# Kernel optimization log

Measured on AMD Instinct MI355X. Metric: run time of the kernel, lower is better.

Reference implementation:

```python
import jax, jax.numpy as jnp
import numpy as np

B, D, C = 8192, 2048, 1000
EPS32 = float(np.finfo(np.float32).eps)      # torch clamp_probs uses finfo.eps
LOG_2PI = float(np.log(2.0 * np.pi))
GAMMA = float(1.0 / np.exp(100.0))           # lerp at global_step=0 -> start_val = 1/exp(start_rho)


def setup_inputs() -> dict:
    key = jax.random.key(0)
    k = jax.random.split(key, 6)
    feature = jax.random.normal(k[0], (B, D), jnp.float32)
    target = jax.random.randint(k[1], (B,), 0, C)
    eps = jax.random.normal(k[2], (B, D), jnp.float32)
    # y_project: Linear(C, D) -> weight [D, C], bias [D]
    y_w = jax.random.normal(k[3], (D, C), jnp.float32) * 0.02
    y_b = jnp.zeros((D,), jnp.float32)
    # cls_project: Linear(D, C) -> weight [C, D], bias [C]
    # small weights + positive bias keep Categorical probs positive (torch would
    # clamp negatives to eps; we replicate the clamp but avoid degenerate NaNs)
    cls_w = jax.random.normal(k[4], (C, D), jnp.float32) * 0.001
    cls_b = jnp.ones((C,), jnp.float32) * 5.0
    return dict(feature=feature, y_w=y_w, y_b=y_b, cls_w=cls_w, cls_b=cls_b,
                eps=eps, target=target)


def reference(feature, y_w, y_b, cls_w, cls_b, eps, target):
    # z = m.sample() : identity-covariance MVN sample, detached (torch .sample())
    z = jax.lax.stop_gradient(feature + eps)                      # [B, D]

    # y_emb = y_project(one_hot(target)) == gather of weight columns + bias
    y_emb = jnp.take(y_w, target, axis=1).T + y_b                 # [B, D]

    # Categorical(probs=cls_project(z)): normalize, clamp, log
    probs_raw = z @ cls_w.T + cls_b                               # [B, C]
    p = probs_raw / jnp.sum(probs_raw, axis=-1, keepdims=True)
    logits = jnp.log(jnp.clip(p, EPS32, 1.0 - EPS32))             # [B, C]

    # identity-covariance MVN log_prob in closed form
    const = 0.5 * D * LOG_2PI
    h1 = 0.5 * jnp.sum((z - feature) ** 2, axis=-1) + const       # -m.log_prob(z)
    h2 = 0.5 * jnp.sum((z - y_emb) ** 2, axis=-1) + const         # -y_emb_d.log_prob(z)
    h3 = -jnp.take_along_axis(logits, target[:, None], axis=1)[:, 0]

    rex = h2 - h1
    loss = jnp.mean(jnp.float32(GAMMA) * rex + h3)
    return logits, loss
```

## Files before the change

kernel.cpp:

```cpp
#include <hip/hip_runtime.h>
#include <hip/hip_bf16.h>

#define B_ROWS 8192
#define D_DIM  2048
#define C_DIM  1000
#define C_PAD  1024

#define EPS32   1.1920928955078125e-07f
#define GAMMA_F 3.7200759760208361e-44f

typedef __attribute__((ext_vector_type(8))) short short8;
typedef __attribute__((ext_vector_type(4))) float f32x4;

#define GLOAD_LDS16(gptr, lptr) \
  __builtin_amdgcn_global_load_lds((const __attribute__((address_space(1))) void*)(gptr), \
                                   (__attribute__((address_space(3))) void*)(lptr), 16, 0, 0)

__device__ inline unsigned short f2bf(float x) {
  union { __hip_bfloat16 b; unsigned short u; } cv;
  cv.b = __float2bfloat16(x);
  return cv.u;
}

__device__ inline float wave_red(float v) {
#pragma unroll
  for (int off = 32; off > 0; off >>= 1) v += __shfl_down(v, off, 64);
  return v;
}

__global__ __launch_bounds__(256) void prep(const float* __restrict__ cls_w,
                                            const float* __restrict__ y_w,
                                            const float* __restrict__ y_b,
                                            __hip_bfloat16* __restrict__ clsw_bf,
                                            float* __restrict__ ywtb) {
  __shared__ float tile[32][33];
  int bid = blockIdx.x;
  if (bid < 1024) {
    int j = (bid * 256 + threadIdx.x) * 8;
    int row = j >> 11;
    int col = j & 2047;
    union { unsigned short u[8]; uint4 v; } pk;
    if (row < C_DIM) {
      const float* src = cls_w + (size_t)row * D_DIM + col;
#pragma unroll
      for (int i = 0; i < 8; ++i) pk.u[i] = f2bf(src[i]);
    } else {
#pragma unroll
      for (int i = 0; i < 8; ++i) pk.u[i] = 0;
    }
    *(uint4*)((unsigned short*)clsw_bf + j) = pk.v;
  } else {
    int b2 = bid - 1024;
    int tb = b2 & 31, db = b2 >> 5;
    int t0 = tb * 32, d0 = db * 32;
    int tx = threadIdx.x & 31, ty = threadIdx.x >> 5;
#pragma unroll
    for (int r = 0; r < 4; ++r) {
      int d = d0 + ty + r * 8;
      int t = t0 + tx;
      tile[ty + r * 8][tx] = (t < C_DIM) ? y_w[(size_t)d * C_DIM + t] : 0.f;
    }
    __syncthreads();
#pragma unroll
    for (int r = 0; r < 4; ++r) {
      int t = t0 + ty + r * 8;
      int d = d0 + tx;
      if (t < C_DIM) ywtb[(size_t)t * D_DIM + d] = tile[tx][ty + r * 8] + y_b[d];
    }
  }
}

__global__ __launch_bounds__(256) void fuse_z(const float* __restrict__ feature,
                                              const float* __restrict__ eps,
                                              const float* __restrict__ ywtb,
                                              const int* __restrict__ target,
                                              __hip_bfloat16* __restrict__ z_bf,
                                              float* __restrict__ rex) {
  int b = blockIdx.x;
  int tid = threadIdx.x;
  int t = target[b];
  const float4* f4 = (const float4*)(feature + (size_t)b * D_DIM);
  const float4* e4 = (const float4*)(eps + (size_t)b * D_DIM);
  const float4* y4 = (const float4*)(ywtb + (size_t)t * D_DIM);
  uint2* zrow = (uint2*)((unsigned short*)z_bf + (size_t)b * D_DIM);

  float se = 0.f, sd = 0.f;
#pragma unroll
  for (int i = 0; i < 2; ++i) {
    int idx = tid + i * 256;
    float4 f = f4[idx];
    float4 e = e4[idx];
    float4 y = y4[idx];
    float z0 = f.x + e.x, z1 = f.y + e.y, z2 = f.z + e.z, z3 = f.w + e.w;
    union { unsigned short u[4]; uint2 v; } pz;
    pz.u[0] = f2bf(z0); pz.u[1] = f2bf(z1); pz.u[2] = f2bf(z2); pz.u[3] = f2bf(z3);
    zrow[idx] = pz.v;
    float a0 = z0 - f.x, a1 = z1 - f.y, a2 = z2 - f.z, a3 = z3 - f.w;
    se += a0 * a0 + a1 * a1 + a2 * a2 + a3 * a3;
    float g0 = z0 - y.x, g1 = z1 - y.y, g2 = z2 - y.z, g3 = z3 - y.w;
    sd += g0 * g0 + g1 * g1 + g2 * g2 + g3 * g3;
  }
  se = wave_red(se);
  sd = wave_red(sd);
  __shared__ float s1[4], s2[4];
  int lane = tid & 63, w = tid >> 6;
  if (lane == 0) { s1[w] = se; s2[w] = sd; }
  __syncthreads();
  if (tid == 0) {
    float S1 = s1[0] + s1[1] + s1[2] + s1[3];
    float S2 = s2[0] + s2[1] + s2[2] + s2[3];
    rex[b] = 0.5f * (S2 - S1);
  }
}

__global__ __launch_bounds__(256) void gemm_bt(const __hip_bfloat16* __restrict__ A,
                                               const __hip_bfloat16* __restrict__ Bt,
                                               const float* __restrict__ cls_b,
                                               float* __restrict__ out) {
  __shared__ __align__(16) __hip_bfloat16 sA[64 * 64];
  __shared__ __align__(16) __hip_bfloat16 sB[128 * 64];
  const int tid = threadIdx.x;
  const int m0 = blockIdx.x * 64;
  const int n0 = blockIdx.y * 128;
  const int w = tid >> 6, lane = tid & 63;
  const int wn = w * 32;
  const int l15 = lane & 15, quad = lane >> 4;

  f32x4 acc[4][2] = {};

  for (int k0 = 0; k0 < D_DIM; k0 += 64) {
#pragma unroll
    for (int i = 0; i < 2; ++i) {
      int j = i * 256 + tid;
      int row = j >> 3, cc = j & 7;
      GLOAD_LDS16(A + (size_t)(m0 + row) * D_DIM + k0 + cc * 8, &sA[j * 8]);
    }
#pragma unroll
    for (int i = 0; i < 4; ++i) {
      int j = i * 256 + tid;
      int row = j >> 3, cc = j & 7;
      GLOAD_LDS16(Bt + (size_t)(n0 + row) * D_DIM + k0 + cc * 8, &sB[j * 8]);
    }
    __syncthreads();
#pragma unroll
    for (int kk = 0; kk < 64; kk += 32) {
      short8 af[4], bfr[2];
#pragma unroll
      for (int i = 0; i < 4; ++i)
        af[i] = *(const short8*)&sA[(i * 16 + l15) * 64 + kk + quad * 8];
#pragma unroll
      for (int jn = 0; jn < 2; ++jn)
        bfr[jn] = *(const short8*)&sB[(wn + jn * 16 + l15) * 64 + kk + quad * 8];
#pragma unroll
      for (int i = 0; i < 4; ++i)
#pragma unroll
        for (int jn = 0; jn < 2; ++jn)
          acc[i][jn] = __builtin_amdgcn_mfma_f32_16x16x32_bf16(af[i], bfr[jn], acc[i][jn], 0, 0, 0);
    }
    __syncthreads();
  }

#pragma unroll
  for (int i = 0; i < 4; ++i) {
    int row = m0 + i * 16 + quad * 4;
#pragma unroll
    for (int jn = 0; jn < 2; ++jn) {
      int col = n0 + wn + jn * 16 + l15;
      if (col < C_DIM) {
        float bias = cls_b[col];
#pragma unroll
        for (int r = 0; r < 4; ++r)
          out[(size_t)(row + r) * C_DIM + col] = acc[i][jn][r] + bias;
      }
    }
  }
}

__global__ __launch_bounds__(256) void rownorm(float* __restrict__ out,
                                               const int* __restrict__ target,
                                               float* __restrict__ rowloss) {
  int b = blockIdx.x, tid = threadIdx.x;
  float* row = out + (size_t)b * C_DIM;
  float v[4];
  float s = 0.f;
#pragma unroll
  for (int i = 0; i < 4; ++i) {
    int c = tid + i * 256;
    v[i] = (c < C_DIM) ? row[c] : 0.f;
    s += v[i];
  }
  s = wave_red(s);
  __shared__ float ws_[4];
  __shared__ float h3s;
  int lane = tid & 63, w = tid >> 6;
  if (lane == 0) ws_[w] = s;
  __syncthreads();
  float total = ws_[0] + ws_[1] + ws_[2] + ws_[3];
  float inv = 1.0f / total;
  int t = target[b];
#pragma unroll
  for (int i = 0; i < 4; ++i) {
    int c = tid + i * 256;
    if (c < C_DIM) {
      float p = v[i] * inv;
      p = fminf(fmaxf(p, EPS32), 1.0f - EPS32);
      float lg = __logf(p);
      row[c] = lg;
      if (c == t) h3s = -lg;
    }
  }
  __syncthreads();
  if (tid == 0) {
    float rx = rowloss[b];
    rowloss[b] = fmaf(GAMMA_F, rx, h3s);
  }
}

__global__ __launch_bounds__(256) void finalize(const float* __restrict__ rowloss,
                                                float* __restrict__ out_loss) {
  int tid = threadIdx.x;
  float s = 0.f;
  for (int i = tid; i < B_ROWS; i += 256) s += rowloss[i];
  s = wave_red(s);
  __shared__ float sm[4];
  if ((tid & 63) == 0) sm[tid >> 6] = s;
  __syncthreads();
  if (tid == 0) out_loss[0] = (sm[0] + sm[1] + sm[2] + sm[3]) * (1.0f / B_ROWS);
}

extern "C" void kernel_launch(void* const* d_in, const int* in_sizes, int n_in,
                              void* d_out, int out_size, void* d_ws, size_t ws_size,
                              hipStream_t stream) {
  const float* feature = (const float*)d_in[0];
  const float* y_w     = (const float*)d_in[1];
  const float* y_b     = (const float*)d_in[2];
  const float* cls_w   = (const float*)d_in[3];
  const float* cls_b   = (const float*)d_in[4];
  const float* eps     = (const float*)d_in[5];
  const int*   target  = (const int*)d_in[6];
  float* out = (float*)d_out;

  char* ws = (char*)d_ws;
  __hip_bfloat16* z_bf    = (__hip_bfloat16*)ws;
  __hip_bfloat16* clsw_bf = (__hip_bfloat16*)(ws + 33554432);
  float*          ywtb    = (float*)(ws + 33554432 + 4194304);
  float*          rex     = (float*)(ws + 33554432 + 4194304 + 8192000);

  prep<<<dim3(1024 + 2048), 256, 0, stream>>>(cls_w, y_w, y_b, clsw_bf, ywtb);
  fuse_z<<<dim3(B_ROWS), 256, 0, stream>>>(feature, eps, ywtb, target, z_bf, rex);
  gemm_bt<<<dim3(B_ROWS / 64, C_PAD / 128), 256, 0, stream>>>(z_bf, clsw_bf, cls_b, out);
  rownorm<<<dim3(B_ROWS), 256, 0, stream>>>(out, target, rex);
  finalize<<<dim3(1), 256, 0, stream>>>(rex, out + (size_t)B_ROWS * C_DIM);
}
```

Measured before the change: 262.1 us.

## Enlarge GEMM tile to 128x128 with XOR-swizzled LDS and atomic loss reduction

The GEMM block tile grows from 64x128 to 128x128, with each of the four waves computing a 64x64 sub-tile (4x4 MFMAs). This raises MFMA work per LDS fragment load and halves the number of blocks. LDS chunks are XOR-swizzled by row to cut bank conflicts on the short8 fragment reads. The separate finalize kernel is removed: rownorm atomically adds each row's scaled loss into the output, which prep zeroes first. This saves a launch but makes the float summation order nondeterministic.

```diff
diff --git a/kernel.cpp b/kernel.cpp
--- a/kernel.cpp
+++ b/kernel.cpp
@@ -32,9 +32,11 @@
                                             const float* __restrict__ y_w,
                                             const float* __restrict__ y_b,
                                             __hip_bfloat16* __restrict__ clsw_bf,
-                                            float* __restrict__ ywtb) {
+                                            float* __restrict__ ywtb,
+                                            float* __restrict__ out_loss) {
   __shared__ float tile[32][33];
   int bid = blockIdx.x;
+  if (bid == 0 && threadIdx.x == 0) out_loss[0] = 0.f;
   if (bid < 1024) {
     int j = (bid * 256 + threadIdx.x) * 8;
     int row = j >> 11;
@@ -117,44 +119,47 @@
                                                const __hip_bfloat16* __restrict__ Bt,
                                                const float* __restrict__ cls_b,
                                                float* __restrict__ out) {
-  __shared__ __align__(16) __hip_bfloat16 sA[64 * 64];
+  __shared__ __align__(16) __hip_bfloat16 sA[128 * 64];
   __shared__ __align__(16) __hip_bfloat16 sB[128 * 64];
   const int tid = threadIdx.x;
-  const int m0 = blockIdx.x * 64;
+  const int m0 = blockIdx.x * 128;
   const int n0 = blockIdx.y * 128;
   const int w = tid >> 6, lane = tid & 63;
-  const int wn = w * 32;
+  const int wm = (w & 1) * 64, wn = (w >> 1) * 64;
   const int l15 = lane & 15, quad = lane >> 4;
 
-  f32x4 acc[4][2] = {};
+  f32x4 acc[4][4] = {};
 
   for (int k0 = 0; k0 < D_DIM; k0 += 64) {
-#pragma unroll
-    for (int i = 0; i < 2; ++i) {
-      int j = i * 256 + tid;
-      int row = j >> 3, cc = j & 7;
-      GLOAD_LDS16(A + (size_t)(m0 + row) * D_DIM + k0 + cc * 8, &sA[j * 8]);
-    }
 #pragma unroll
     for (int i = 0; i < 4; ++i) {
       int j = i * 256 + tid;
-      int row = j >> 3, cc = j & 7;
-      GLOAD_LDS16(Bt + (size_t)(n0 + row) * D_DIM + k0 + cc * 8, &sB[j * 8]);
+      int row = j >> 3;
+      int cc = (j & 7) ^ (row & 7);
+      const __hip_bfloat16* srcA = A + (size_t)(m0 + row) * D_DIM + k0 + cc * 8;
+      const __hip_bfloat16* srcB = Bt + (size_t)(n0 + row) * D_DIM + k0 + cc * 8;
+      GLOAD_LDS16(srcA, &sA[j * 8]);
+      GLOAD_LDS16(srcB, &sB[j * 8]);
     }
     __syncthreads();
 #pragma unroll
     for (int kk = 0; kk < 64; kk += 32) {
-      short8 af[4], bfr[2];
+      const int ccr = (kk >> 3) + quad;
+      short8 af[4], bfr[4];
+#pragma unroll
+      for (int i = 0; i < 4; ++i) {
+        int r = wm + i * 16 + l15;
+        af[i] = *(const short8*)&sA[(r * 8 + (ccr ^ (r & 7))) * 8];
+      }
+#pragma unroll
+      for (int jn = 0; jn < 4; ++jn) {
+        int r = wn + jn * 16 + l15;
+        bfr[jn] = *(const short8*)&sB[(r * 8 + (ccr ^ (r & 7))) * 8];
+      }
 #pragma unroll
       for (int i = 0; i < 4; ++i)
-        af[i] = *(const short8*)&sA[(i * 16 + l15) * 64 + kk + quad * 8];
-#pragma unroll
-      for (int jn = 0; jn < 2; ++jn)
-        bfr[jn] = *(const short8*)&sB[(wn + jn * 16 + l15) * 64 + kk + quad * 8];
-#pragma unroll
-      for (int i = 0; i < 4; ++i)
-#pragma unroll
-        for (int jn = 0; jn < 2; ++jn)
+#pragma unroll
+        for (int jn = 0; jn < 4; ++jn)
           acc[i][jn] = __builtin_amdgcn_mfma_f32_16x16x32_bf16(af[i], bfr[jn], acc[i][jn], 0, 0, 0);
     }
     __syncthreads();
@@ -162,9 +167,9 @@
 
 #pragma unroll
   for (int i = 0; i < 4; ++i) {
-    int row = m0 + i * 16 + quad * 4;
-#pragma unroll
-    for (int jn = 0; jn < 2; ++jn) {
+    int row = m0 + wm + i * 16 + quad * 4;
+#pragma unroll
+    for (int jn = 0; jn < 4; ++jn) {
       int col = n0 + wn + jn * 16 + l15;
       if (col < C_DIM) {
         float bias = cls_b[col];
@@ -178,7 +183,8 @@
 
 __global__ __launch_bounds__(256) void rownorm(float* __restrict__ out,
                                                const int* __restrict__ target,
-                                               float* __restrict__ rowloss) {
+                                               const float* __restrict__ rex,
+                                               float* __restrict__ out_loss) {
   int b = blockIdx.x, tid = threadIdx.x;
   float* row = out + (size_t)b * C_DIM;
   float v[4];
@@ -211,21 +217,9 @@
   }
   __syncthreads();
   if (tid == 0) {
-    float rx = rowloss[b];
-    rowloss[b] = fmaf(GAMMA_F, rx, h3s);
-  }
-}
-
-__global__ __launch_bounds__(256) void finalize(const float* __restrict__ rowloss,
-                                                float* __restrict__ out_loss) {
-  int tid = threadIdx.x;
-  float s = 0.f;
-  for (int i = tid; i < B_ROWS; i += 256) s += rowloss[i];
-  s = wave_red(s);
-  __shared__ float sm[4];
-  if ((tid & 63) == 0) sm[tid >> 6] = s;
-  __syncthreads();
-  if (tid == 0) out_loss[0] = (sm[0] + sm[1] + sm[2] + sm[3]) * (1.0f / B_ROWS);
+    float rowloss = fmaf(GAMMA_F, rex[b], h3s);
+    atomicAdd(out_loss, rowloss * (1.0f / B_ROWS));
+  }
 }
 
 extern "C" void kernel_launch(void* const* d_in, const int* in_sizes, int n_in,
@@ -239,6 +233,7 @@
   const float* eps     = (const float*)d_in[5];
   const int*   target  = (const int*)d_in[6];
   float* out = (float*)d_out;
+  float* out_loss = out + (size_t)B_ROWS * C_DIM;
 
   char* ws = (char*)d_ws;
   __hip_bfloat16* z_bf    = (__hip_bfloat16*)ws;
@@ -246,9 +241,8 @@
   float*          ywtb    = (float*)(ws + 33554432 + 4194304);
   float*          rex     = (float*)(ws + 33554432 + 4194304 + 8192000);
 
-  prep<<<dim3(1024 + 2048), 256, 0, stream>>>(cls_w, y_w, y_b, clsw_bf, ywtb);
+  prep<<<dim3(1024 + 2048), 256, 0, stream>>>(cls_w, y_w, y_b, clsw_bf, ywtb, out_loss);
   fuse_z<<<dim3(B_ROWS), 256, 0, stream>>>(feature, eps, ywtb, target, z_bf, rex);
-  gemm_bt<<<dim3(B_ROWS / 64, C_PAD / 128), 256, 0, stream>>>(z_bf, clsw_bf, cls_b, out);
-  rownorm<<<dim3(B_ROWS), 256, 0, stream>>>(out, target, rex);
-  finalize<<<dim3(1), 256, 0, stream>>>(rex, out + (size_t)B_ROWS * C_DIM);
-}
+  gemm_bt<<<dim3(B_ROWS / 128, C_PAD / 128), 256, 0, stream>>>(z_bf, clsw_bf, cls_b, out);
+  rownorm<<<dim3(B_ROWS), 256, 0, stream>>>(out, target, rex, out_loss);
+}
```

After: 336.0 us. 1.28x slower.
